# Optimization experiments

Hardware: AMD Instinct MI355X
Metric: run time of the kernel (lower is better)

## Reference

```python
import jax, jax.numpy as jnp
import numpy as np

B, N, E, H = 8, 512, 128, 64


def setup_inputs() -> dict:
    key = jax.random.key(0)
    k1, k2, k3 = jax.random.split(key, 3)
    h_freq = jax.random.normal(k1, (B * N, E), dtype=jnp.float32)
    W = jax.random.normal(k2, (2 * E, H), dtype=jnp.float32) * 0.05  # Linear(2E -> H) weight, stored input-major
    b = jnp.zeros((H,), dtype=jnp.float32)
    att = jax.random.normal(k3, (H,), dtype=jnp.float32) * 0.1
    return {"h_freq": h_freq, "W": W, "b": b, "att": att, "batch": B, "n_nodes": N}


def reference(h_freq, W, b, att, batch, n_nodes):
    n = n_nodes
    bsz = h_freq.shape[0] // n
    h = h_freq.reshape(bsz, n, -1)  # [B, N, E]
    # Fused form of cat([hj, hk]) @ W: split W into the hj-half and hk-half.
    W1, W2 = W[: h.shape[-1]], W[h.shape[-1]:]
    pj = h @ W1  # [B, N, H]
    pk = h @ W2  # [B, N, H]
    u = jax.nn.leaky_relu(pj[:, :, None, :] + pk[:, None, :, :] + b, negative_slope=0.2)  # [B, N, N, H]
    e = jnp.einsum("bjkh,h->bjk", u, att)  # [B, N, N]
    alpha = jax.nn.softmax(e, axis=2)
    # dense_to_sparse with learn_sys=True: symmetrize, drop diagonal (eval mode: no dropout)
    dense = (alpha + jnp.swapaxes(alpha, -1, -2)) * 0.5
    mask = ~np.eye(n, dtype=bool)
    src, dst = np.nonzero(mask)  # static, length n*(n-1)
    src = jnp.asarray(src, dtype=jnp.int64)
    dst = jnp.asarray(dst, dtype=jnp.int64)
    single = jnp.stack([src, dst], axis=0)  # [2, M]
    offsets = (jnp.arange(bsz, dtype=jnp.int64) * n)
    edge_index = (single[:, None, :] + offsets[None, :, None]).reshape(2, -1)  # [2, B*M]
    edge_weights = dense[:, src, dst].reshape(-1)  # [B*M]
    return edge_index, edge_weights, alpha
```

## Files before the change

kernel.cpp:

```cpp
#include <hip/hip_runtime.h>
#include <hip/hip_bf16.h>

#define BB 8
#define NN 512
#define EE 128
#define HH 64
#define EP (NN * (NN - 1))
#define ECNT (BB * EP)
#define OFF_EI0 0
#define OFF_EI1 ECNT
#define OFF_EW  (2 * ECNT)
#define OFF_AL  (3 * ECNT)

__global__ __launch_bounds__(256) void k_proj(
        const float* __restrict__ h, const float* __restrict__ W,
        const float* __restrict__ bvec, const float* __restrict__ att,
        float* __restrict__ pj, float* __restrict__ pkT,
        float* __restrict__ cj, float* __restrict__ dk) {
    const int row0 = blockIdx.x * 8;
    const int tid  = threadIdx.x;
    const int c    = tid & 63;
    const int w    = __builtin_amdgcn_readfirstlane(tid >> 6);

    const float* hA = h + (size_t)(row0 + w) * EE;
    const float* hB = h + (size_t)(row0 + w + 4) * EE;

    float aj0 = 0.f, ak0 = 0.f, aj1 = 0.f, ak1 = 0.f;
#pragma unroll
    for (int e = 0; e < EE; ++e) {
        const float w1 = W[e * HH + c];
        const float w2 = W[(EE + e) * HH + c];
        const float h0 = hA[e];
        const float h1 = hB[e];
        aj0 = fmaf(h0, w1, aj0);
        ak0 = fmaf(h0, w2, ak0);
        aj1 = fmaf(h1, w1, aj1);
        ak1 = fmaf(h1, w2, ak1);
    }
    const float bb = bvec[c];
    aj0 += bb; aj1 += bb;

    const float a6 = 0.6f * att[c];

    const int iA = row0 + w;
    const int iB = row0 + w + 4;
    pj[iA * HH + c] = aj0;
    pj[iB * HH + c] = aj1;
    {
        const int bA = iA >> 9, nA = iA & 511;
        const int bB = iB >> 9, nB = iB & 511;
        pkT[((size_t)bA * HH + c) * NN + nA] = ak0;
        pkT[((size_t)bB * HH + c) * NN + nB] = ak1;
    }
    float c0 = a6 * aj0, d0 = a6 * ak0, c1 = a6 * aj1, d1 = a6 * ak1;
#pragma unroll
    for (int off = 32; off >= 1; off >>= 1) {
        c0 += __shfl_xor(c0, off, 64);
        d0 += __shfl_xor(d0, off, 64);
        c1 += __shfl_xor(c1, off, 64);
        d1 += __shfl_xor(d1, off, 64);
    }
    if (c == 0) {
        cj[iA] = c0; dk[iA] = d0;
        cj[iB] = c1; dk[iB] = d1;
    }
}

__global__ __launch_bounds__(512, 4) void k_attn(
        const float* __restrict__ pj, const float* __restrict__ pkT,
        const float* __restrict__ att, const float* __restrict__ cj,
        const float* __restrict__ dk, float* __restrict__ alpha) {
    const int bid   = blockIdx.x;
    const int b     = bid >> 6;
    const int jbase = (bid & 63) * 8;
    const int tid   = threadIdx.x;
    const int lane  = tid & 63;
    const int wid   = tid >> 6;

    __shared__ float e_s[8][NN];

    float pkr[HH];
    const float* pkb = pkT + (size_t)b * HH * NN + tid;
#pragma unroll
    for (int hh = 0; hh < HH; ++hh) pkr[hh] = pkb[hh * NN];
    const float dkv = dk[b * NN + tid];

    const float* pjb = pj + ((size_t)b * NN + jbase) * HH;
    const float* cjb = cj + b * NN + jbase;

    float acc[8];
#pragma unroll
    for (int j = 0; j < 8; ++j) acc[j] = 0.f;

#pragma unroll
    for (int q = 0; q < HH / 4; ++q) {
        const float a0 = att[4 * q + 0];
        const float a1 = att[4 * q + 1];
        const float a2 = att[4 * q + 2];
        const float a3 = att[4 * q + 3];
        const float k0 = pkr[4 * q + 0];
        const float k1 = pkr[4 * q + 1];
        const float k2 = pkr[4 * q + 2];
        const float k3 = pkr[4 * q + 3];
#pragma unroll
        for (int j = 0; j < 8; ++j) {
            const float p0 = pjb[j * HH + 4 * q + 0];
            const float p1 = pjb[j * HH + 4 * q + 1];
            const float p2 = pjb[j * HH + 4 * q + 2];
            const float p3 = pjb[j * HH + 4 * q + 3];
            float s;
            s = p0 + k0; acc[j] = fmaf(a0, fabsf(s), acc[j]);
            s = p1 + k1; acc[j] = fmaf(a1, fabsf(s), acc[j]);
            s = p2 + k2; acc[j] = fmaf(a2, fabsf(s), acc[j]);
            s = p3 + k3; acc[j] = fmaf(a3, fabsf(s), acc[j]);
        }
    }

#pragma unroll
    for (int j = 0; j < 8; ++j)
        e_s[j][tid] = fmaf(0.4f, acc[j], cjb[j] + dkv);
    __syncthreads();

    {
        float v[8];
        float m = -1e30f;
#pragma unroll
        for (int i2 = 0; i2 < 8; ++i2) {
            v[i2] = e_s[wid][lane + 64 * i2];
            m = fmaxf(m, v[i2]);
        }
#pragma unroll
        for (int off = 32; off >= 1; off >>= 1) m = fmaxf(m, __shfl_xor(m, off, 64));
        float s = 0.f;
#pragma unroll
        for (int i2 = 0; i2 < 8; ++i2) { v[i2] = __expf(v[i2] - m); s += v[i2]; }
#pragma unroll
        for (int off = 32; off >= 1; off >>= 1) s += __shfl_xor(s, off, 64);
        const float inv = 1.0f / s;
        float* arow = alpha + ((size_t)b * NN + jbase + wid) * NN;
#pragma unroll
        for (int i2 = 0; i2 < 8; ++i2) arow[lane + 64 * i2] = v[i2] * inv;
    }
}

__global__ void k_edges(const float* __restrict__ alpha, float* __restrict__ out) {
    const int bid   = blockIdx.x;
    const int b     = bid >> 6;
    const int jt    = (bid >> 3) & 7;
    const int kt    = bid & 7;
    const int jbase = jt * 64;
    const int kbase = kt * 64;
    const int tid   = threadIdx.x;
    const int c     = tid & 63;
    const int r0    = tid >> 6;

    __shared__ float at[64][65];

    const float* A = alpha + (size_t)b * NN * NN;

#pragma unroll
    for (int i = 0; i < 16; ++i) {
        const int r = i * 4 + r0;
        at[c][r] = A[(kbase + r) * NN + jbase + c];
    }
    __syncthreads();

    const float fb = (float)(b * NN);
#pragma unroll
    for (int i = 0; i < 16; ++i) {
        const int jj = i * 4 + r0;
        const int j  = jbase + jj;
        const int k  = kbase + c;
        if (k == j) continue;
        const float w = 0.5f * (A[j * NN + k] + at[jj][c]);
        const unsigned t   = (unsigned)k - ((k > j) ? 1u : 0u);
        const unsigned idx = (unsigned)b * EP + (unsigned)j * (NN - 1) + t;
        out[OFF_EI0 + idx] = fb + (float)j;
        out[OFF_EI1 + idx] = fb + (float)k;
        out[OFF_EW  + idx] = w;
    }
}

extern "C" void kernel_launch(void* const* d_in, const int* in_sizes, int n_in,
                              void* d_out, int out_size, void* d_ws, size_t ws_size,
                              hipStream_t stream) {
    const float* h    = (const float*)d_in[0];
    const float* W    = (const float*)d_in[1];
    const float* bvec = (const float*)d_in[2];
    const float* att  = (const float*)d_in[3];
    float* out = (float*)d_out;

    float* pj  = (float*)d_ws;
    float* pkT = pj + (size_t)BB * NN * HH;
    float* cj  = pkT + (size_t)BB * NN * HH;
    float* dk  = cj + BB * NN;

    float* alpha = out + OFF_AL;

    k_proj <<<BB * NN / 8, 256, 0, stream>>>(h, W, bvec, att, pj, pkT, cj, dk);
    k_attn <<<BB * 64, 512, 0, stream>>>(pj, pkT, att, cj, dk, alpha);
    k_edges<<<BB * 64, 256, 0, stream>>>(alpha, out);
}
```

Measured before the change: 39.97 us.

## Stage W and pj in LDS and process symmetric tile pairs in edge kernel

```diff
diff --git a/kernel.cpp b/kernel.cpp
--- a/kernel.cpp
+++ b/kernel.cpp
@@ -17,19 +17,28 @@
         const float* __restrict__ bvec, const float* __restrict__ att,
         float* __restrict__ pj, float* __restrict__ pkT,
         float* __restrict__ cj, float* __restrict__ dk) {
+    __shared__ float Wl[2 * EE * HH];
+    const int tid = threadIdx.x;
+
+    {
+        float4* Wl4 = reinterpret_cast<float4*>(Wl);
+        const float4* W4 = reinterpret_cast<const float4*>(W);
+#pragma unroll
+        for (int r = 0; r < 16; ++r) Wl4[r * 256 + tid] = W4[r * 256 + tid];
+    }
+
     const int row0 = blockIdx.x * 8;
-    const int tid  = threadIdx.x;
-    const int c    = tid & 63;
-    const int w    = __builtin_amdgcn_readfirstlane(tid >> 6);
-
+    const int c = tid & 63;
+    const int w = tid >> 6;
     const float* hA = h + (size_t)(row0 + w) * EE;
     const float* hB = h + (size_t)(row0 + w + 4) * EE;
+    __syncthreads();
 
     float aj0 = 0.f, ak0 = 0.f, aj1 = 0.f, ak1 = 0.f;
 #pragma unroll
     for (int e = 0; e < EE; ++e) {
-        const float w1 = W[e * HH + c];
-        const float w2 = W[(EE + e) * HH + c];
+        const float w1 = Wl[e * HH + c];
+        const float w2 = Wl[(EE + e) * HH + c];
         const float h0 = hA[e];
         const float h1 = hB[e];
         aj0 = fmaf(h0, w1, aj0);
@@ -41,7 +50,6 @@
     aj0 += bb; aj1 += bb;
 
     const float a6 = 0.6f * att[c];
-
     const int iA = row0 + w;
     const int iB = row0 + w + 4;
     pj[iA * HH + c] = aj0;
@@ -77,42 +85,43 @@
     const int lane  = tid & 63;
     const int wid   = tid >> 6;
 
-    __shared__ float e_s[8][NN];
+    __shared__ float4 pj4[8][HH / 4];
+    __shared__ float  e_s[8][NN];
+
+    if (tid < 128) {
+        const int j = tid >> 4, q = tid & 15;
+        pj4[j][q] = reinterpret_cast<const float4*>(
+            pj + ((size_t)b * NN + jbase + j) * HH)[q];
+    }
 
     float pkr[HH];
     const float* pkb = pkT + (size_t)b * HH * NN + tid;
 #pragma unroll
     for (int hh = 0; hh < HH; ++hh) pkr[hh] = pkb[hh * NN];
     const float dkv = dk[b * NN + tid];
-
-    const float* pjb = pj + ((size_t)b * NN + jbase) * HH;
     const float* cjb = cj + b * NN + jbase;
 
+    __syncthreads();
+
     float acc[8];
 #pragma unroll
     for (int j = 0; j < 8; ++j) acc[j] = 0.f;
 
 #pragma unroll
     for (int q = 0; q < HH / 4; ++q) {
-        const float a0 = att[4 * q + 0];
-        const float a1 = att[4 * q + 1];
-        const float a2 = att[4 * q + 2];
-        const float a3 = att[4 * q + 3];
+        const float4 af = reinterpret_cast<const float4*>(att)[q];
         const float k0 = pkr[4 * q + 0];
         const float k1 = pkr[4 * q + 1];
         const float k2 = pkr[4 * q + 2];
         const float k3 = pkr[4 * q + 3];
 #pragma unroll
         for (int j = 0; j < 8; ++j) {
-            const float p0 = pjb[j * HH + 4 * q + 0];
-            const float p1 = pjb[j * HH + 4 * q + 1];
-            const float p2 = pjb[j * HH + 4 * q + 2];
-            const float p3 = pjb[j * HH + 4 * q + 3];
+            const float4 pw = pj4[j][q];
             float s;
-            s = p0 + k0; acc[j] = fmaf(a0, fabsf(s), acc[j]);
-            s = p1 + k1; acc[j] = fmaf(a1, fabsf(s), acc[j]);
-            s = p2 + k2; acc[j] = fmaf(a2, fabsf(s), acc[j]);
-            s = p3 + k3; acc[j] = fmaf(a3, fabsf(s), acc[j]);
+            s = pw.x + k0; acc[j] = fmaf(af.x, fabsf(s), acc[j]);
+            s = pw.y + k1; acc[j] = fmaf(af.y, fabsf(s), acc[j]);
+            s = pw.z + k2; acc[j] = fmaf(af.z, fabsf(s), acc[j]);
+            s = pw.w + k3; acc[j] = fmaf(af.w, fabsf(s), acc[j]);
         }
     }
 
@@ -144,40 +153,69 @@
 }
 
 __global__ void k_edges(const float* __restrict__ alpha, float* __restrict__ out) {
-    const int bid   = blockIdx.x;
-    const int b     = bid >> 6;
-    const int jt    = (bid >> 3) & 7;
-    const int kt    = bid & 7;
+    const int bid = blockIdx.x;
+    const int b   = bid / 36;
+    int rem = bid - b * 36;
+    int jt = 0;
+    while (rem >= 8 - jt) { rem -= 8 - jt; ++jt; }
+    const int kt = jt + rem;
+
     const int jbase = jt * 64;
     const int kbase = kt * 64;
     const int tid   = threadIdx.x;
     const int c     = tid & 63;
     const int r0    = tid >> 6;
 
-    __shared__ float at[64][65];
+    __shared__ float t1[64][65];
+    __shared__ float t2[64][65];
 
     const float* A = alpha + (size_t)b * NN * NN;
+    const bool diag = (jt == kt);
 
 #pragma unroll
     for (int i = 0; i < 16; ++i) {
         const int r = i * 4 + r0;
-        at[c][r] = A[(kbase + r) * NN + jbase + c];
+        t1[r][c] = A[(size_t)(jbase + r) * NN + kbase + c];
+    }
+    if (!diag) {
+#pragma unroll
+        for (int i = 0; i < 16; ++i) {
+            const int r = i * 4 + r0;
+            t2[r][c] = A[(size_t)(kbase + r) * NN + jbase + c];
+        }
     }
     __syncthreads();
 
     const float fb = (float)(b * NN);
+
 #pragma unroll
     for (int i = 0; i < 16; ++i) {
         const int jj = i * 4 + r0;
         const int j  = jbase + jj;
         const int k  = kbase + c;
         if (k == j) continue;
-        const float w = 0.5f * (A[j * NN + k] + at[jj][c]);
+        const float a_kj = diag ? t1[c][jj] : t2[c][jj];
+        const float wv = 0.5f * (t1[jj][c] + a_kj);
         const unsigned t   = (unsigned)k - ((k > j) ? 1u : 0u);
         const unsigned idx = (unsigned)b * EP + (unsigned)j * (NN - 1) + t;
         out[OFF_EI0 + idx] = fb + (float)j;
         out[OFF_EI1 + idx] = fb + (float)k;
-        out[OFF_EW  + idx] = w;
+        out[OFF_EW  + idx] = wv;
+    }
+
+    if (!diag) {
+#pragma unroll
+        for (int i = 0; i < 16; ++i) {
+            const int kk = i * 4 + r0;
+            const int j2 = kbase + kk;
+            const int k2 = jbase + c;
+            const float wv = 0.5f * (t2[kk][c] + t1[c][kk]);
+            const unsigned t   = (unsigned)k2 - ((k2 > j2) ? 1u : 0u);
+            const unsigned idx = (unsigned)b * EP + (unsigned)j2 * (NN - 1) + t;
+            out[OFF_EI0 + idx] = fb + (float)j2;
+            out[OFF_EI1 + idx] = fb + (float)k2;
+            out[OFF_EW  + idx] = wv;
+        }
     }
 }
 
@@ -199,5 +237,5 @@
 
     k_proj <<<BB * NN / 8, 256, 0, stream>>>(h, W, bvec, att, pj, pkT, cj, dk);
     k_attn <<<BB * 64, 512, 0, stream>>>(pj, pkT, att, cj, dk, alpha);
-    k_edges<<<BB * 64, 256, 0, stream>>>(alpha, out);
-}
+    k_edges<<<BB * 36, 256, 0, stream>>>(alpha, out);
+}
```

Result: slower. 41.82 us (+4.6%).
